# Performance work log

Hardware: AMD Instinct MI355X
Metric: run time of the kernel (lower is better)

## Reference

```python
import jax, jax.numpy as jnp
import numpy as np

N, M = 8192, 4096
SCALE = 1e-4  # keeps tss ~ O(1) so the gaussian score doesn't underflow


def setup_inputs() -> dict:
    key = jax.random.key(0)
    x = jax.random.normal(key, (N, M), dtype=jnp.float32) * SCALE
    variance = jnp.asarray(0.9, dtype=jnp.float32)
    return {"x": x, "variance": variance}


def reference(x, variance):
    # _lpd vectorized over all columns at once.
    # series_a/series_b are first differences with a leading zero row; the
    # leading zeros contribute 0 to the sum (0*0>=0 -> 0-0), so we can work
    # directly on the diffs.
    d = jnp.diff(x, axis=0)                 # [N-1, M]
    da = d[:, :1]                           # reference column diffs [N-1, 1]
    db = d[:, 1:]                           # other column diffs    [N-1, M-1]
    diff = da - db
    hpdd = jnp.where(da * db >= 0, diff, jnp.abs(diff))
    tss = jnp.sum(hpdd, axis=0)             # [M-1]
    # torch.tensor(self.tss) detaches tss from x's autograd graph
    tss = jax.lax.stop_gradient(tss)

    # gaussian score with mean 0, sigma = variance
    sqrt_2pi = jnp.sqrt(jnp.asarray(2.0 * np.pi, dtype=x.dtype))
    coef = 1.0 / (sqrt_2pi * variance)
    score = coef * jnp.exp(-(tss ** 2) / (2.0 * variance ** 2))  # [M-1]

    # tan-softmax weighting
    t = jnp.tan(score)
    w = t / jnp.sum(t)                      # [M-1]

    y = jnp.reshape(jnp.sum(w * x[:, 1:]), (-1,))  # [1]
    return y
```

## Files before the change

### kernel.cpp

```cpp
#include <hip/hip_runtime.h>
#include <math.h>

#define NROWS 8192
#define NCOLS 4096
#define RPC 32
#define NCHUNK (NROWS / RPC)
#define TPB 1024
#define CPT 4
#define F2BLK 256
#define TPB2 1024
#define CPB2 (NCOLS / F2BLK)
#define PARTS2 64

typedef float f32x4 __attribute__((ext_vector_type(4)));

__global__ __launch_bounds__(TPB) void tss_partial_kernel(
    const float* __restrict__ x,
    float* __restrict__ ptss,
    float* __restrict__ pcs)
{
    const int tid   = threadIdx.x;
    const int chunk = blockIdx.x;
    const int col   = tid * CPT;
    const int r0    = chunk * RPC;

    __shared__ float x0[RPC + 1];
    __shared__ float da_sh[RPC];

    if (tid <= RPC) {
        int r = min(r0 + tid, NROWS - 1);
        x0[tid] = x[(size_t)r * NCOLS];
    }
    __syncthreads();
    if (tid < RPC) {
        da_sh[tid] = (r0 + tid + 1 < NROWS) ? (x0[tid + 1] - x0[tid]) : 0.0f;
    }
    __syncthreads();

    const f32x4* row = (const f32x4*)(x + (size_t)r0 * NCOLS + col);
    const int rs = NCOLS / 4;
    const int maxoff = NROWS - 1 - r0;

    float tss0 = 0.f, tss1 = 0.f, tss2 = 0.f, tss3 = 0.f;
    float cs0 = 0.f, cs1 = 0.f, cs2 = 0.f, cs3 = 0.f;

    f32x4 cur = row[0];
    f32x4 nxt = row[min(1, maxoff) * rs];

    #pragma unroll 8
    for (int i = 0; i < RPC; ++i) {
        const int offc = (i + 2 <= RPC) ? (i + 2) : RPC;
        const int off  = min(offc, maxoff);
        f32x4 pf = row[off * rs];

        cs0 += cur.x; cs1 += cur.y; cs2 += cur.z; cs3 += cur.w;

        const float da = da_sh[i];
        float db, df;
        db = nxt.x - cur.x; df = da - db;
        tss0 += (da * db >= 0.f) ? df : fabsf(df);
        db = nxt.y - cur.y; df = da - db;
        tss1 += (da * db >= 0.f) ? df : fabsf(df);
        db = nxt.z - cur.z; df = da - db;
        tss2 += (da * db >= 0.f) ? df : fabsf(df);
        db = nxt.w - cur.w; df = da - db;
        tss3 += (da * db >= 0.f) ? df : fabsf(df);

        cur = nxt;
        nxt = pf;
    }

    float* pt = ptss + (size_t)chunk * NCOLS + col;
    float* pc = pcs  + (size_t)chunk * NCOLS + col;
    *(f32x4*)pt = (f32x4){tss0, tss1, tss2, tss3};
    *(f32x4*)pc = (f32x4){cs0, cs1, cs2, cs3};
}

__global__ __launch_bounds__(TPB2) void tss_finalize_kernel(
    const float* __restrict__ ptss,
    const float* __restrict__ pcs,
    const float* __restrict__ variance,
    double* __restrict__ blk)
{
    const int tid  = threadIdx.x;
    const int cg   = tid & 15;
    const int part = tid >> 4;
    const int j    = blockIdx.x * CPB2 + cg;

    double tss = 0.0, cs = 0.0;
    const int c0 = part * (NCHUNK / PARTS2);
    #pragma unroll
    for (int k = 0; k < NCHUNK / PARTS2; ++k) {
        const int c = c0 + k;
        tss += (double)ptss[(size_t)c * NCOLS + j];
        cs  += (double)pcs[(size_t)c * NCOLS + j];
    }

    __shared__ double stss[PARTS2][CPB2 + 1];
    __shared__ double scs[PARTS2][CPB2 + 1];
    stss[part][cg] = tss;
    scs[part][cg]  = cs;
    __syncthreads();

    for (int s = PARTS2 / 2; s >= 1; s >>= 1) {
        if (part < s) {
            stss[part][cg] += stss[part + s][cg];
            scs[part][cg]  += scs[part + s][cg];
        }
        __syncthreads();
    }

    if (tid < CPB2) {
        const double tssT = stss[0][tid];
        const double csT  = scs[0][tid];

        double t = 0.0, tc = 0.0;
        const int jj = blockIdx.x * CPB2 + tid;
        if (jj >= 1) {
            const double var = (double)variance[0];
            const double SQRT_2PI = 2.5066282746310005024;
            const double coef = 1.0 / (SQRT_2PI * var);
            const double score = coef * exp(-(tssT * tssT) / (2.0 * var * var));
            t  = tan(score);
            tc = t * csT;
        }
        for (int o = 8; o > 0; o >>= 1) {
            t  += __shfl_down(t, o);
            tc += __shfl_down(tc, o);
        }
        if (tid == 0) {
            blk[2 * blockIdx.x]     = t;
            blk[2 * blockIdx.x + 1] = tc;
        }
    }
}

__global__ __launch_bounds__(64) void tss_reduce_kernel(
    const double* __restrict__ blk,
    float* __restrict__ out)
{
    const int tid = threadIdx.x;
    double st = 0.0, stc = 0.0;
    #pragma unroll
    for (int k = 0; k < F2BLK / 64; ++k) {
        st  += blk[2 * (tid + 64 * k)];
        stc += blk[2 * (tid + 64 * k) + 1];
    }
    for (int o = 32; o > 0; o >>= 1) {
        st  += __shfl_down(st, o);
        stc += __shfl_down(stc, o);
    }
    if (tid == 0) out[0] = (float)(stc / st);
}

extern "C" void kernel_launch(void* const* d_in, const int* in_sizes, int n_in,
                              void* d_out, int out_size, void* d_ws, size_t ws_size,
                              hipStream_t stream) {
    const float* x   = (const float*)d_in[0];
    const float* var = (const float*)d_in[1];
    float* out = (float*)d_out;

    float* ptss = (float*)d_ws;
    float* pcs  = ptss + (size_t)NCHUNK * NCOLS;
    double* blk = (double*)(pcs + (size_t)NCHUNK * NCOLS);

    tss_partial_kernel<<<NCHUNK, TPB, 0, stream>>>(x, ptss, pcs);
    tss_finalize_kernel<<<F2BLK, TPB2, 0, stream>>>(ptss, pcs, var, blk);
    tss_reduce_kernel<<<1, 64, 0, stream>>>(blk, out);
}
```

Measured before the change: 33.04 us.

## Fuse three reduction kernels into one cooperative kernel with grid syncs

Merges the partial, finalize and final-reduce kernels into a single cooperative launch of 256 blocks that uses grid.sync() between the phases, removing two kernel launch gaps. The per-chunk reference-column diffs now live in registers and are broadcast with wave shuffles, replacing the shared-memory staging and two __syncthreads. The cost is two grid-wide barriers. It also depends on all 256 blocks of 1024 threads being co-resident, which cooperative launch requires.

Measured after the change: 101.0 us. 206% more time.

```diff
diff --git a/kernel.cpp b/kernel.cpp
--- a/kernel.cpp
+++ b/kernel.cpp
@@ -1,5 +1,8 @@
 #include <hip/hip_runtime.h>
+#include <hip/hip_cooperative_groups.h>
 #include <math.h>
+
+namespace cg = cooperative_groups;
 
 #define NROWS 8192
 #define NCOLS 4096
@@ -7,150 +10,145 @@
 #define NCHUNK (NROWS / RPC)
 #define TPB 1024
 #define CPT 4
-#define F2BLK 256
-#define TPB2 1024
-#define CPB2 (NCOLS / F2BLK)
+#define CPB2 (NCOLS / NCHUNK)
 #define PARTS2 64
 
 typedef float f32x4 __attribute__((ext_vector_type(4)));
 
-__global__ __launch_bounds__(TPB) void tss_partial_kernel(
+__global__ __launch_bounds__(TPB) void tss_fused_kernel(
     const float* __restrict__ x,
     float* __restrict__ ptss,
-    float* __restrict__ pcs)
+    float* __restrict__ pcs,
+    const float* __restrict__ variance,
+    double* __restrict__ blk,
+    float* __restrict__ out)
 {
-    const int tid   = threadIdx.x;
-    const int chunk = blockIdx.x;
-    const int col   = tid * CPT;
-    const int r0    = chunk * RPC;
+    cg::grid_group grid = cg::this_grid();
+    const int tid = threadIdx.x;
 
-    __shared__ float x0[RPC + 1];
-    __shared__ float da_sh[RPC];
+    {
+        const int chunk = blockIdx.x;
+        const int col   = tid * CPT;
+        const int r0    = chunk * RPC;
+        const int lane  = tid & 63;
 
-    if (tid <= RPC) {
-        int r = min(r0 + tid, NROWS - 1);
-        x0[tid] = x[(size_t)r * NCOLS];
-    }
-    __syncthreads();
-    if (tid < RPC) {
-        da_sh[tid] = (r0 + tid + 1 < NROWS) ? (x0[tid + 1] - x0[tid]) : 0.0f;
-    }
-    __syncthreads();
+        float x0v = 0.f;
+        {
+            const int r = min(r0 + lane, NROWS - 1);
+            if (lane <= RPC) x0v = x[(size_t)r * NCOLS];
+        }
+        const float xnx = __shfl_down(x0v, 1);
+        const float da_reg = (lane < RPC && (r0 + lane + 1 < NROWS)) ? (xnx - x0v) : 0.f;
 
-    const f32x4* row = (const f32x4*)(x + (size_t)r0 * NCOLS + col);
-    const int rs = NCOLS / 4;
-    const int maxoff = NROWS - 1 - r0;
+        const f32x4* row = (const f32x4*)(x + (size_t)r0 * NCOLS + col);
+        const int rs = NCOLS / 4;
+        const int maxoff = NROWS - 1 - r0;
 
-    float tss0 = 0.f, tss1 = 0.f, tss2 = 0.f, tss3 = 0.f;
-    float cs0 = 0.f, cs1 = 0.f, cs2 = 0.f, cs3 = 0.f;
+        float tss0 = 0.f, tss1 = 0.f, tss2 = 0.f, tss3 = 0.f;
+        float cs0 = 0.f, cs1 = 0.f, cs2 = 0.f, cs3 = 0.f;
 
-    f32x4 cur = row[0];
-    f32x4 nxt = row[min(1, maxoff) * rs];
+        f32x4 cur = row[0];
+        f32x4 nxt = row[min(1, maxoff) * rs];
 
-    #pragma unroll 8
-    for (int i = 0; i < RPC; ++i) {
-        const int offc = (i + 2 <= RPC) ? (i + 2) : RPC;
-        const int off  = min(offc, maxoff);
-        f32x4 pf = row[off * rs];
+        #pragma unroll 8
+        for (int i = 0; i < RPC; ++i) {
+            const int offc = (i + 2 <= RPC) ? (i + 2) : RPC;
+            const int off  = min(offc, maxoff);
+            f32x4 pf = row[off * rs];
 
-        cs0 += cur.x; cs1 += cur.y; cs2 += cur.z; cs3 += cur.w;
+            cs0 += cur.x; cs1 += cur.y; cs2 += cur.z; cs3 += cur.w;
 
-        const float da = da_sh[i];
-        float db, df;
-        db = nxt.x - cur.x; df = da - db;
-        tss0 += (da * db >= 0.f) ? df : fabsf(df);
-        db = nxt.y - cur.y; df = da - db;
-        tss1 += (da * db >= 0.f) ? df : fabsf(df);
-        db = nxt.z - cur.z; df = da - db;
-        tss2 += (da * db >= 0.f) ? df : fabsf(df);
-        db = nxt.w - cur.w; df = da - db;
-        tss3 += (da * db >= 0.f) ? df : fabsf(df);
+            const float da = __shfl(da_reg, i);
+            float db, df;
+            db = nxt.x - cur.x; df = da - db;
+            tss0 += (da * db >= 0.f) ? df : fabsf(df);
+            db = nxt.y - cur.y; df = da - db;
+            tss1 += (da * db >= 0.f) ? df : fabsf(df);
+            db = nxt.z - cur.z; df = da - db;
+            tss2 += (da * db >= 0.f) ? df : fabsf(df);
+            db = nxt.w - cur.w; df = da - db;
+            tss3 += (da * db >= 0.f) ? df : fabsf(df);
 
-        cur = nxt;
-        nxt = pf;
+            cur = nxt;
+            nxt = pf;
+        }
+
+        float* pt = ptss + (size_t)chunk * NCOLS + col;
+        float* pc = pcs  + (size_t)chunk * NCOLS + col;
+        *(f32x4*)pt = (f32x4){tss0, tss1, tss2, tss3};
+        *(f32x4*)pc = (f32x4){cs0, cs1, cs2, cs3};
     }
 
-    float* pt = ptss + (size_t)chunk * NCOLS + col;
-    float* pc = pcs  + (size_t)chunk * NCOLS + col;
-    *(f32x4*)pt = (f32x4){tss0, tss1, tss2, tss3};
-    *(f32x4*)pc = (f32x4){cs0, cs1, cs2, cs3};
-}
+    grid.sync();
 
-__global__ __launch_bounds__(TPB2) void tss_finalize_kernel(
-    const float* __restrict__ ptss,
-    const float* __restrict__ pcs,
-    const float* __restrict__ variance,
-    double* __restrict__ blk)
-{
-    const int tid  = threadIdx.x;
-    const int cg   = tid & 15;
-    const int part = tid >> 4;
-    const int j    = blockIdx.x * CPB2 + cg;
+    {
+        const int cg_  = tid & 15;
+        const int part = tid >> 4;
+        const int j    = blockIdx.x * CPB2 + cg_;
 
-    double tss = 0.0, cs = 0.0;
-    const int c0 = part * (NCHUNK / PARTS2);
-    #pragma unroll
-    for (int k = 0; k < NCHUNK / PARTS2; ++k) {
-        const int c = c0 + k;
-        tss += (double)ptss[(size_t)c * NCOLS + j];
-        cs  += (double)pcs[(size_t)c * NCOLS + j];
+        double tss = 0.0, cs = 0.0;
+        const int c0 = part * (NCHUNK / PARTS2);
+        #pragma unroll
+        for (int k = 0; k < NCHUNK / PARTS2; ++k) {
+            const int c = c0 + k;
+            tss += (double)ptss[(size_t)c * NCOLS + j];
+            cs  += (double)pcs[(size_t)c * NCOLS + j];
+        }
+
+        __shared__ double stss[PARTS2][CPB2 + 1];
+        __shared__ double scs[PARTS2][CPB2 + 1];
+        stss[part][cg_] = tss;
+        scs[part][cg_]  = cs;
+        __syncthreads();
+
+        for (int s = PARTS2 / 2; s >= 1; s >>= 1) {
+            if (part < s) {
+                stss[part][cg_] += stss[part + s][cg_];
+                scs[part][cg_]  += scs[part + s][cg_];
+            }
+            __syncthreads();
+        }
+
+        if (tid < CPB2) {
+            const double tssT = stss[0][tid];
+            const double csT  = scs[0][tid];
+
+            double t = 0.0, tc = 0.0;
+            const int jj = blockIdx.x * CPB2 + tid;
+            if (jj >= 1) {
+                const double var = (double)variance[0];
+                const double SQRT_2PI = 2.5066282746310005024;
+                const double coef = 1.0 / (SQRT_2PI * var);
+                const double score = coef * exp(-(tssT * tssT) / (2.0 * var * var));
+                t  = tan(score);
+                tc = t * csT;
+            }
+            for (int o = 8; o > 0; o >>= 1) {
+                t  += __shfl_down(t, o);
+                tc += __shfl_down(tc, o);
+            }
+            if (tid == 0) {
+                blk[2 * blockIdx.x]     = t;
+                blk[2 * blockIdx.x + 1] = tc;
+            }
+        }
     }
 
-    __shared__ double stss[PARTS2][CPB2 + 1];
-    __shared__ double scs[PARTS2][CPB2 + 1];
-    stss[part][cg] = tss;
-    scs[part][cg]  = cs;
-    __syncthreads();
+    grid.sync();
 
-    for (int s = PARTS2 / 2; s >= 1; s >>= 1) {
-        if (part < s) {
-            stss[part][cg] += stss[part + s][cg];
-            scs[part][cg]  += scs[part + s][cg];
+    if (blockIdx.x == 0 && tid < 64) {
+        double st = 0.0, stc = 0.0;
+        #pragma unroll
+        for (int k = 0; k < NCHUNK / 64; ++k) {
+            st  += blk[2 * (tid + 64 * k)];
+            stc += blk[2 * (tid + 64 * k) + 1];
         }
-        __syncthreads();
+        for (int o = 32; o > 0; o >>= 1) {
+            st  += __shfl_down(st, o);
+            stc += __shfl_down(stc, o);
+        }
+        if (tid == 0) out[0] = (float)(stc / st);
     }
-
-    if (tid < CPB2) {
-        const double tssT = stss[0][tid];
-        const double csT  = scs[0][tid];
-
-        double t = 0.0, tc = 0.0;
-        const int jj = blockIdx.x * CPB2 + tid;
-        if (jj >= 1) {
-            const double var = (double)variance[0];
-            const double SQRT_2PI = 2.5066282746310005024;
-            const double coef = 1.0 / (SQRT_2PI * var);
-            const double score = coef * exp(-(tssT * tssT) / (2.0 * var * var));
-            t  = tan(score);
-            tc = t * csT;
-        }
-        for (int o = 8; o > 0; o >>= 1) {
-            t  += __shfl_down(t, o);
-            tc += __shfl_down(tc, o);
-        }
-        if (tid == 0) {
-            blk[2 * blockIdx.x]     = t;
-            blk[2 * blockIdx.x + 1] = tc;
-        }
-    }
-}
-
-__global__ __launch_bounds__(64) void tss_reduce_kernel(
-    const double* __restrict__ blk,
-    float* __restrict__ out)
-{
-    const int tid = threadIdx.x;
-    double st = 0.0, stc = 0.0;
-    #pragma unroll
-    for (int k = 0; k < F2BLK / 64; ++k) {
-        st  += blk[2 * (tid + 64 * k)];
-        stc += blk[2 * (tid + 64 * k) + 1];
-    }
-    for (int o = 32; o > 0; o >>= 1) {
-        st  += __shfl_down(st, o);
-        stc += __shfl_down(stc, o);
-    }
-    if (tid == 0) out[0] = (float)(stc / st);
 }
 
 extern "C" void kernel_launch(void* const* d_in, const int* in_sizes, int n_in,
@@ -164,7 +162,8 @@
     float* pcs  = ptss + (size_t)NCHUNK * NCOLS;
     double* blk = (double*)(pcs + (size_t)NCHUNK * NCOLS);
 
-    tss_partial_kernel<<<NCHUNK, TPB, 0, stream>>>(x, ptss, pcs);
-    tss_finalize_kernel<<<F2BLK, TPB2, 0, stream>>>(ptss, pcs, var, blk);
-    tss_reduce_kernel<<<1, 64, 0, stream>>>(blk, out);
+    void* args[] = {(void*)&x, (void*)&ptss, (void*)&pcs, (void*)&var,
+                    (void*)&blk, (void*)&out};
+    hipLaunchCooperativeKernel((void*)tss_fused_kernel, dim3(NCHUNK), dim3(TPB),
+                               args, 0, stream);
 }
```
